# Kernel optimization log

Hardware: AMD Instinct MI355X
Metric: run time of the kernel (lower is better)

Reference implementation:

```python
import jax, jax.numpy as jnp
import numpy as np

D_MODEL = 4096
D_FF = 11008
M = 8192
GROUP = 128
NLEVELS = 16  # 4-bit


def setup_inputs() -> dict:
    key = jax.random.key(0)
    ks = jax.random.split(key, 10)
    def qw(k, K, N):
        return jax.random.randint(k, (K, N), 0, NLEVELS, dtype=jnp.int32)
    def qz(k, G, N):
        return jax.random.randint(k, (G, N), 0, NLEVELS, dtype=jnp.int32)
    def sc(k, G, N):
        # small positive per-group scales, roughly matching real AWQ magnitudes
        return jax.random.uniform(k, (G, N), dtype=jnp.float32) * 0.02 + 1e-3
    return {
        "x": jax.random.normal(ks[0], (M, D_MODEL), dtype=jnp.float32),
        "q_gate": qw(ks[1], D_MODEL, D_FF),
        "z_gate": qz(ks[2], D_MODEL // GROUP, D_FF),
        "s_gate": sc(ks[3], D_MODEL // GROUP, D_FF),
        "q_up": qw(ks[4], D_MODEL, D_FF),
        "z_up": qz(ks[5], D_MODEL // GROUP, D_FF),
        "s_up": sc(ks[6], D_MODEL // GROUP, D_FF),
        "q_down": qw(ks[7], D_FF, D_MODEL),
        "z_down": qz(ks[8], D_FF // GROUP, D_MODEL),
        "s_down": sc(ks[9], D_FF // GROUP, D_MODEL),
        "group_size": GROUP,
    }


def _dequant(q, z, s, group_size):
    # q: [K, N] int4 values; z: [K//G, N] zeros; s: [K//G, N] scales
    K, N = q.shape
    G = group_size
    w = (q.astype(s.dtype).reshape(K // G, G, N) - z.astype(s.dtype)[:, None, :]) * s[:, None, :]
    return w.reshape(K, N)


def reference(x, q_gate, z_gate, s_gate, q_up, z_up, s_up, q_down, z_down, s_down, group_size):
    gate = x @ _dequant(q_gate, z_gate, s_gate, group_size)   # [M, D_FF]
    up = x @ _dequant(q_up, z_up, s_up, group_size)           # [M, D_FF]
    h = jax.nn.silu(gate) * up                                # SwiGLU
    return h @ _dequant(q_down, z_down, s_down, group_size)   # [M, D_MODEL]
```

## Files before the change

kernel.cpp:

```cpp
#include <hip/hip_runtime.h>
#include <cstdint>

typedef unsigned short u16;
typedef unsigned int u32;
typedef unsigned char u8;
typedef signed char s8;
typedef __bf16 bf16_t;
typedef bf16_t bf16x8 __attribute__((ext_vector_type(8)));
typedef float f32x4 __attribute__((ext_vector_type(4)));
typedef int i32x4 __attribute__((ext_vector_type(4)));

#define DMODEL 4096
#define DFF 11008
#define MROWS 8192

__device__ __forceinline__ u16 f2bf(float f) {
  u32 u = __builtin_bit_cast(u32, f);
  u += 0x7FFFu + ((u >> 16) & 1u);
  return (u16)(u >> 16);
}
__device__ __forceinline__ float bf2f(u16 h) {
  return __builtin_bit_cast(float, (u32)h << 16);
}

#define GLD16(gptr, lptr)                                                  \
  __builtin_amdgcn_global_load_lds(                                        \
      (const __attribute__((address_space(1))) u32*)(gptr),                \
      (__attribute__((address_space(3))) u32*)(lptr), 16, 0, 0)

#define BAR asm volatile("s_barrier" ::: "memory")
#define VM0 asm volatile("s_waitcnt vmcnt(0)" ::: "memory")
#define VM4 asm volatile("s_waitcnt vmcnt(4)" ::: "memory")
#define LGKM0 asm volatile("s_waitcnt lgkmcnt(0)" ::: "memory")

__global__ void k_quant_x(const float* __restrict__ x, s8* __restrict__ x8,
                          float* __restrict__ sx) {
  const int row = blockIdx.x;
  const int t = threadIdx.x;
  const int lane = t & 63, wid = t >> 6;
  const float4* xr = reinterpret_cast<const float4*>(x + (size_t)row * DMODEL);
  float4 v[4];
  float m = 0.f;
#pragma unroll
  for (int i = 0; i < 4; ++i) {
    v[i] = xr[t * 4 + i];
    m = fmaxf(m, fmaxf(fmaxf(fabsf(v[i].x), fabsf(v[i].y)),
                       fmaxf(fabsf(v[i].z), fabsf(v[i].w))));
  }
#pragma unroll
  for (int off = 32; off >= 1; off >>= 1) m = fmaxf(m, __shfl_xor(m, off));
  __shared__ float wm[4];
  if (lane == 0) wm[wid] = m;
  __syncthreads();
  float mall = fmaxf(fmaxf(wm[0], wm[1]), fmaxf(wm[2], wm[3]));
  mall = fmaxf(mall, 1e-8f);
  const float inv = 127.f / mall;
  if (t == 0) sx[row] = mall / 127.f;
  uint4 o;
  u32 p[4];
#pragma unroll
  for (int i = 0; i < 4; ++i) {
    int a = (int)rintf(v[i].x * inv), b = (int)rintf(v[i].y * inv);
    int c = (int)rintf(v[i].z * inv), d = (int)rintf(v[i].w * inv);
    p[i] = (u32)(a & 255) | ((u32)(b & 255) << 8) | ((u32)(c & 255) << 16) |
           ((u32)(d & 255) << 24);
  }
  o.x = p[0]; o.y = p[1]; o.z = p[2]; o.w = p[3];
  reinterpret_cast<uint4*>(x8 + (size_t)row * DMODEL)[t] = o;
}

__global__ void k_dequant_T8(const int* __restrict__ q, const int* __restrict__ z,
                             s8* __restrict__ w8, int K, int N) {
  __shared__ s8 tile[32][40];
  const int t = threadIdx.x;
  const int n0 = blockIdx.x << 5, k0 = blockIdx.y << 5;
  {
    const int kr = t >> 3, n4 = (t & 7) << 2;
    const int k = k0 + kr, g = k >> 7;
    const int4 qv = *reinterpret_cast<const int4*>(&q[(size_t)k * N + n0 + n4]);
    const int4 zv = *reinterpret_cast<const int4*>(&z[(size_t)g * N + n0 + n4]);
    tile[kr][n4 + 0] = (s8)(qv.x - zv.x);
    tile[kr][n4 + 1] = (s8)(qv.y - zv.y);
    tile[kr][n4 + 2] = (s8)(qv.z - zv.z);
    tile[kr][n4 + 3] = (s8)(qv.w - zv.w);
  }
  __syncthreads();
  {
    const int n = t >> 3, ks = (t & 7) << 2;
    uchar4 o;
    o.x = (u8)tile[ks + 0][n];
    o.y = (u8)tile[ks + 1][n];
    o.z = (u8)tile[ks + 2][n];
    o.w = (u8)tile[ks + 3][n];
    *reinterpret_cast<uchar4*>(&w8[(size_t)(n0 + n) * K + k0 + ks]) = o;
  }
}

__global__ void k_dequant_T(const int* __restrict__ q, const int* __restrict__ z,
                            const float* __restrict__ s, u16* __restrict__ wT,
                            int K, int N) {
  __shared__ u16 tile[32][36];
  const int t = threadIdx.x;
  const int n0 = blockIdx.x << 5, k0 = blockIdx.y << 5;
  {
    const int kr = t >> 3, n4 = (t & 7) << 2;
    const int k = k0 + kr, g = k >> 7;
    const int4 qv = *reinterpret_cast<const int4*>(&q[(size_t)k * N + n0 + n4]);
    const int4 zv = *reinterpret_cast<const int4*>(&z[(size_t)g * N + n0 + n4]);
    const float4 sv = *reinterpret_cast<const float4*>(&s[(size_t)g * N + n0 + n4]);
    ushort4 o;
    o.x = f2bf((float)(qv.x - zv.x) * sv.x);
    o.y = f2bf((float)(qv.y - zv.y) * sv.y);
    o.z = f2bf((float)(qv.z - zv.z) * sv.z);
    o.w = f2bf((float)(qv.w - zv.w) * sv.w);
    *reinterpret_cast<ushort4*>(&tile[kr][n4]) = o;
  }
  __syncthreads();
  {
    const int n = t >> 3, ks = (t & 7) << 2;
    ushort4 o;
    o.x = tile[ks + 0][n];
    o.y = tile[ks + 1][n];
    o.z = tile[ks + 2][n];
    o.w = tile[ks + 3][n];
    *reinterpret_cast<ushort4*>(&wT[(size_t)(n0 + n) * K + k0 + ks]) = o;
  }
}

__global__ __launch_bounds__(512, 2) void k_fused_i8(
    const s8* __restrict__ A, const s8* __restrict__ Bg,
    const s8* __restrict__ Bu, const float* __restrict__ sx,
    const float* __restrict__ sg, const float* __restrict__ su,
    u16* __restrict__ H) {
  constexpr int Kdim = DMODEL;
  constexpr int ntiles = Kdim >> 6;
  __shared__ s8 Ab[3][256 * 64];
  __shared__ s8 Bgb[3][128 * 64];
  __shared__ s8 Bub[3][128 * 64];
  __shared__ float scl[2][32 * 128];

  const int midx = blockIdx.x & 31, nidx = blockIdx.x >> 5;
  const int m0 = midx << 8, n0 = nidx << 7;
  const int t = threadIdx.x;
  const int lane = t & 63;
  const int wid = t >> 6;
  const int wr = wid >> 2, wc = wid & 3;
  const int r16 = lane & 15, quad = lane >> 4;

  const int lrow = lane >> 2;
  const int sswz = ((lane & 3) ^ ((lrow >> 1) & 3)) << 4;
  const s8* Asrc = A + (size_t)(m0 + wid * 16 + lrow) * Kdim + sswz;
  const s8* Gsrc = Bg + (size_t)(n0 + wid * 16 + lrow) * Kdim + sswz;
  const s8* Usrc = Bu + (size_t)(n0 + wid * 16 + lrow) * Kdim + sswz;
  const size_t rstepA = (size_t)128 * Kdim;
  const int ldst = wid * 1024;

#define STG(tt, bs) do {                                                   \
    size_t ko = (size_t)((tt) & (ntiles - 1)) << 6;                        \
    GLD16(Asrc + ko,          &Ab[bs][ldst]);                              \
    GLD16(Asrc + ko + rstepA, &Ab[bs][ldst + 8192]);                       \
    GLD16(Gsrc + ko,          &Bgb[bs][ldst]);                             \
    GLD16(Usrc + ko,          &Bub[bs][ldst]);                             \
  } while (0)

  const int aswz = (quad ^ ((r16 >> 1) & 3)) << 4;
  const int abase = (wr * 128 + r16) * 64 + aswz;
  const int bbase = (wc * 32 + r16) * 64 + aswz;

  f32x4 facg[8][2], facu[8][2];
  const f32x4 zf = {0.f, 0.f, 0.f, 0.f};
#pragma unroll
  for (int mf = 0; mf < 8; ++mf)
#pragma unroll
    for (int nf = 0; nf < 2; ++nf) { facg[mf][nf] = zf; facu[mf][nf] = zf; }
  const i32x4 zi = {0, 0, 0, 0};

#pragma unroll
  for (int k = 0; k < 2; ++k) {
    int j = t + k * 512;
    int g = j >> 5;
    int c = (j & 31) << 2;
    *reinterpret_cast<float4*>(&scl[0][g * 128 + c]) =
        *reinterpret_cast<const float4*>(&sg[(size_t)g * DFF + n0 + c]);
    *reinterpret_cast<float4*>(&scl[1][g * 128 + c]) =
        *reinterpret_cast<const float4*>(&su[(size_t)g * DFF + n0 + c]);
  }
  STG(0, 0); STG(1, 1);
  VM0;
  LGKM0;
  BAR;

  const int sloc = wc * 32 + r16;

  int cur = 0;
  for (int i = 0; i < (ntiles >> 1); ++i) {
    const int a = cur;
    const int b = (a + 1 < 3) ? a + 1 : a - 2;
    const int c = (a + 2 < 3) ? a + 2 : a - 1;
    i32x4 av0[8], bg_a[2], bg_b[2], bu_a[2], bu_b[2];
#pragma unroll
    for (int mf = 0; mf < 8; ++mf)
      av0[mf] = *reinterpret_cast<const i32x4*>(&Ab[a][abase + mf * 1024]);
#pragma unroll
    for (int nf = 0; nf < 2; ++nf) {
      bg_a[nf] = *reinterpret_cast<const i32x4*>(&Bgb[a][bbase + nf * 1024]);
      bu_a[nf] = *reinterpret_cast<const i32x4*>(&Bub[a][bbase + nf * 1024]);
      bg_b[nf] = *reinterpret_cast<const i32x4*>(&Bgb[b][bbase + nf * 1024]);
      bu_b[nf] = *reinterpret_cast<const i32x4*>(&Bub[b][bbase + nf * 1024]);
    }
    float s_g0 = scl[0][i * 128 + sloc];
    float s_g1 = scl[0][i * 128 + sloc + 16];
    float s_u0 = scl[1][i * 128 + sloc];
    float s_u1 = scl[1][i * 128 + sloc + 16];
    STG(2 * i + 2, c);
    LGKM0;
    BAR;
    STG(2 * i + 3, a);
    __builtin_amdgcn_s_setprio(1);
#pragma unroll
    for (int mf = 0; mf < 8; ++mf) {
      i32x4 a1 = *reinterpret_cast<const i32x4*>(&Ab[b][abase + mf * 1024]);
      i32x4 ig0 = __builtin_amdgcn_mfma_i32_16x16x64_i8(av0[mf], bg_a[0], zi, 0, 0, 0);
      i32x4 ig1 = __builtin_amdgcn_mfma_i32_16x16x64_i8(av0[mf], bg_a[1], zi, 0, 0, 0);
      i32x4 iu0 = __builtin_amdgcn_mfma_i32_16x16x64_i8(av0[mf], bu_a[0], zi, 0, 0, 0);
      i32x4 iu1 = __builtin_amdgcn_mfma_i32_16x16x64_i8(av0[mf], bu_a[1], zi, 0, 0, 0);
      ig0 = __builtin_amdgcn_mfma_i32_16x16x64_i8(a1, bg_b[0], ig0, 0, 0, 0);
      ig1 = __builtin_amdgcn_mfma_i32_16x16x64_i8(a1, bg_b[1], ig1, 0, 0, 0);
      iu0 = __builtin_amdgcn_mfma_i32_16x16x64_i8(a1, bu_b[0], iu0, 0, 0, 0);
      iu1 = __builtin_amdgcn_mfma_i32_16x16x64_i8(a1, bu_b[1], iu1, 0, 0, 0);
#pragma unroll
      for (int j = 0; j < 4; ++j) {
        facg[mf][0][j] += (float)ig0[j] * s_g0;
        facg[mf][1][j] += (float)ig1[j] * s_g1;
        facu[mf][0][j] += (float)iu0[j] * s_u0;
        facu[mf][1][j] += (float)iu1[j] * s_u1;
      }
    }
    __builtin_amdgcn_s_setprio(0);
    VM0;
    BAR;
    cur = c;
  }

  const int rb0 = m0 + wr * 128 + quad * 4;
  const int cb0 = n0 + wc * 32 + r16;
#pragma unroll
  for (int mf = 0; mf < 8; ++mf) {
#pragma unroll
    for (int j = 0; j < 4; ++j) {
      const int row = rb0 + mf * 16 + j;
      const float sxr = sx[row];
#pragma unroll
      for (int nf = 0; nf < 2; ++nf) {
        float gv = facg[mf][nf][j] * sxr;
        float uv = facu[mf][nf][j] * sxr;
        float sv = gv / (1.f + __expf(-gv));
        H[(size_t)row * DFF + cb0 + nf * 16] = f2bf(sv * uv);
      }
    }
  }
#undef STG
}

__global__ __launch_bounds__(512, 2) void k_down(
    const u16* __restrict__ A, const u16* __restrict__ BT,
    float* __restrict__ C) {
  constexpr int Ndim = DMODEL, Kdim = DFF;
  __shared__ u16 As[2][2][256 * 32];
  __shared__ u16 Bs[2][2][256 * 32];

  const int nidx = blockIdx.x & 15;
  const int midx = blockIdx.x >> 4;
  const int m0 = midx << 8;
  const int n0 = nidx << 8;
  const int t = threadIdx.x;
  const int lane = t & 63;
  const int wid = t >> 6;
  const int wr = wid >> 2, wc = wid & 3;
  const int r16 = lane & 15, quad = lane >> 4;

  const int lrow4 = lane >> 2;
  const int sslot = ((lane & 3) ^ ((lane >> 3) & 3)) << 3;
  const u16* Asrc = A + (size_t)(m0 + wid * 16 + lrow4) * Kdim + sslot;
  const u16* Bsrc = BT + (size_t)(n0 + wid * 16 + lrow4) * Kdim + sslot;
  const size_t rstep = (size_t)128 * Kdim;
  const int lbo = wid * 512;
  constexpr int ntiles = Kdim >> 6;

#define SA(tt, kh, bf) do {                                                \
    int ttw = (tt) < ntiles ? (tt) : (tt) - ntiles;                        \
    size_t ko = ((size_t)ttw << 6) + ((kh) << 5);                          \
    GLD16(Asrc + ko,         &As[bf][kh][lbo]);                            \
    GLD16(Asrc + ko + rstep, &As[bf][kh][lbo + 4096]);                     \
  } while (0)
#define SB(tt, kh, bf) do {                                                \
    int ttw = (tt) < ntiles ? (tt) : (tt) - ntiles;                        \
    size_t ko = ((size_t)ttw << 6) + ((kh) << 5);                          \
    GLD16(Bsrc + ko,         &Bs[bf][kh][lbo]);                            \
    GLD16(Bsrc + ko + rstep, &Bs[bf][kh][lbo + 4096]);                     \
  } while (0)

  const int fragoff = (quad ^ ((r16 >> 1) & 3)) << 3;
  const int abase = (wr * 128 + r16) * 32 + fragoff;
  const int bbase = (wc * 64 + r16) * 32 + fragoff;

  f32x4 acc[8][4];
  const f32x4 zf = {0.f, 0.f, 0.f, 0.f};
#pragma unroll
  for (int mf = 0; mf < 8; ++mf)
#pragma unroll
    for (int nf = 0; nf < 4; ++nf) acc[mf][nf] = zf;

  bf16x8 avA[4], av2A[4], bvA[4];
  bf16x8 avB[4], av2B[4], bvB[4];

#define PFD(av_, av2_, bv_, bf, kk) do {                                   \
    _Pragma("unroll") for (int ii = 0; ii < 4; ++ii) {                     \
      av_[ii] = *reinterpret_cast<const bf16x8*>(                          \
          &As[bf][kk][abase + ii * 512]);                                  \
      av2_[ii] = *reinterpret_cast<const bf16x8*>(                         \
          &As[bf][kk][abase + 2048 + ii * 512]);                           \
    }                                                                      \
    _Pragma("unroll") for (int nn = 0; nn < 4; ++nn)                       \
      bv_[nn] = *reinterpret_cast<const bf16x8*>(                          \
          &Bs[bf][kk][bbase + nn * 512]);                                  \
  } while (0)

#define PHD(av_, av2_, bv_, nav_, nav2_, nbv_, STG_, VMW, bfn, kkn) do {   \
    STG_;                                                                  \
    VMW;                                                                   \
    BAR;                                                                   \
    __builtin_amdgcn_s_setprio(1);                                         \
    _Pragma("unroll") for (int ii = 0; ii < 4; ++ii)                       \
      _Pragma("unroll") for (int nn = 0; nn < 4; ++nn)                     \
        acc[ii][nn] = __builtin_amdgcn_mfma_f32_16x16x32_bf16(             \
            av_[ii], bv_[nn], acc[ii][nn], 0, 0, 0);                       \
    PFD(nav_, nav2_, nbv_, bfn, kkn);                                      \
    _Pragma("unroll") for (int ii = 0; ii < 4; ++ii)                       \
      _Pragma("unroll") for (int nn = 0; nn < 4; ++nn)                     \
        acc[4 + ii][nn] = __builtin_amdgcn_mfma_f32_16x16x32_bf16(         \
            av2_[ii], bv_[nn], acc[4 + ii][nn], 0, 0, 0);                  \
    __builtin_amdgcn_s_setprio(0);                                         \
    BAR;                                                                   \
  } while (0)

  SA(0, 0, 0); SB(0, 0, 0); SA(0, 1, 0); SB(0, 1, 0); SA(1, 0, 1); SB(1, 0, 1);
  VM4;
  BAR;
  PFD(avA, av2A, bvA, 0, 0);

  constexpr int NI = ntiles >> 1;
  for (int it = 0; it < NI; ++it) {
    const int t0 = it * 2;
    PHD(avA, av2A, bvA, avB, av2B, bvB,
        { SA(t0 + 1, 1, 1); SB(t0 + 1, 1, 1); }, (void)0, 0, 1);
    PHD(avB, av2B, bvB, avA, av2A, bvA,
        { SA(t0 + 2, 0, 0); SB(t0 + 2, 0, 0); }, VM4, 1, 0);
    PHD(avA, av2A, bvA, avB, av2B, bvB,
        { SA(t0 + 2, 1, 0); SB(t0 + 2, 1, 0); }, (void)0, 1, 1);
    PHD(avB, av2B, bvB, avA, av2A, bvA,
        { SA(t0 + 3, 0, 1); SB(t0 + 3, 0, 1); }, VM4, 0, 0);
  }
  asm volatile("s_waitcnt vmcnt(0)" ::: "memory");

  const int rb0 = m0 + wr * 128 + quad * 4;
  const int cb0 = n0 + wc * 64 + r16;
#pragma unroll
  for (int mf = 0; mf < 8; ++mf) {
#pragma unroll
    for (int nf = 0; nf < 4; ++nf) {
      f32x4 v = acc[mf][nf];
      int row = rb0 + mf * 16;
      int col = cb0 + nf * 16;
#pragma unroll
      for (int j = 0; j < 4; ++j)
        C[(size_t)(row + j) * Ndim + col] = v[j];
    }
  }
#undef SA
#undef SB
#undef PFD
#undef PHD
}

extern "C" void kernel_launch(void* const* d_in, const int* in_sizes, int n_in,
                              void* d_out, int out_size, void* d_ws, size_t ws_size,
                              hipStream_t stream) {
  const float* x  = (const float*)d_in[0];
  const int*   qg = (const int*)d_in[1];
  const int*   zg = (const int*)d_in[2];
  const float* sg = (const float*)d_in[3];
  const int*   qu = (const int*)d_in[4];
  const int*   zu = (const int*)d_in[5];
  const float* su = (const float*)d_in[6];
  const int*   qd = (const int*)d_in[7];
  const int*   zd = (const int*)d_in[8];
  const float* sd = (const float*)d_in[9];
  float* out = (float*)d_out;

  char* ws = (char*)d_ws;
  const size_t szX8 = (size_t)MROWS * DMODEL;
  const size_t szSX = (size_t)MROWS * 4;
  const size_t szW8 = (size_t)DMODEL * DFF;
  const size_t szWD = (size_t)DFF * DMODEL * 2;
  s8*    x8  = (s8*)(ws);
  float* sx  = (float*)(ws + szX8);
  s8*    wg8 = (s8*)(ws + szX8 + szSX);
  s8*    wu8 = (s8*)(ws + szX8 + szSX + szW8);
  u16*   wdT = (u16*)(ws + szX8 + szSX + 2 * szW8);
  u16*   h   = (u16*)(ws + szX8 + szSX + 2 * szW8 + szWD);

  k_quant_x<<<MROWS, 256, 0, stream>>>(x, x8, sx);
  k_dequant_T8<<<dim3(DFF / 32, DMODEL / 32), 256, 0, stream>>>(qg, zg, wg8, DMODEL, DFF);
  k_dequant_T8<<<dim3(DFF / 32, DMODEL / 32), 256, 0, stream>>>(qu, zu, wu8, DMODEL, DFF);
  k_dequant_T<<<dim3(DMODEL / 32, DFF / 32), 256, 0, stream>>>(qd, zd, sd, wdT, DFF, DMODEL);

  k_fused_i8<<<(MROWS / 256) * (DFF / 128), 512, 0, stream>>>(
      x8, wg8, wu8, sx, sg, su, h);
  k_down<<<(MROWS / 256) * (DMODEL / 256), 512, 0, stream>>>(h, wdT, out);
}
```

Before: 2.163 ms.

## Switch fused int8 gate/up kernel to double-buffered tile pairs, bf16 scales

Replaces the 3-slot rotating LDS ring with two ping-pong pairs of K-tiles. Both next tiles are issued at once, which removes the mid-iteration LGKM wait and barrier. Group scales are now stored in LDS as bf16, so the LDS footprint stays within budget for the larger 4-tile buffer. This cuts one barrier per iteration but adds bf16 rounding error on the scales and still uses a lot of LDS, which may limit occupancy.

Measured after the change: 1.824 ms. 1.19x faster.

```diff
diff --git a/kernel.cpp b/kernel.cpp
--- a/kernel.cpp
+++ b/kernel.cpp
@@ -134,10 +134,10 @@
     u16* __restrict__ H) {
   constexpr int Kdim = DMODEL;
   constexpr int ntiles = Kdim >> 6;
-  __shared__ s8 Ab[3][256 * 64];
-  __shared__ s8 Bgb[3][128 * 64];
-  __shared__ s8 Bub[3][128 * 64];
-  __shared__ float scl[2][32 * 128];
+  __shared__ s8 Ab[2][2][256 * 64];
+  __shared__ s8 Bgb[2][2][128 * 64];
+  __shared__ s8 Bub[2][2][128 * 64];
+  __shared__ u16 sclh[2][32 * 128];
 
   const int midx = blockIdx.x & 31, nidx = blockIdx.x >> 5;
   const int m0 = midx << 8, n0 = nidx << 7;
@@ -155,12 +155,12 @@
   const size_t rstepA = (size_t)128 * Kdim;
   const int ldst = wid * 1024;
 
-#define STG(tt, bs) do {                                                   \
+#define STG(tt, pb_, ti) do {                                              \
     size_t ko = (size_t)((tt) & (ntiles - 1)) << 6;                        \
-    GLD16(Asrc + ko,          &Ab[bs][ldst]);                              \
-    GLD16(Asrc + ko + rstepA, &Ab[bs][ldst + 8192]);                       \
-    GLD16(Gsrc + ko,          &Bgb[bs][ldst]);                             \
-    GLD16(Usrc + ko,          &Bub[bs][ldst]);                             \
+    GLD16(Asrc + ko,          &Ab[pb_][ti][ldst]);                         \
+    GLD16(Asrc + ko + rstepA, &Ab[pb_][ti][ldst + 8192]);                  \
+    GLD16(Gsrc + ko,          &Bgb[pb_][ti][ldst]);                        \
+    GLD16(Usrc + ko,          &Bub[pb_][ti][ldst]);                        \
   } while (0)
 
   const int aswz = (quad ^ ((r16 >> 1) & 3)) << 4;
@@ -180,46 +180,44 @@
     int j = t + k * 512;
     int g = j >> 5;
     int c = (j & 31) << 2;
-    *reinterpret_cast<float4*>(&scl[0][g * 128 + c]) =
-        *reinterpret_cast<const float4*>(&sg[(size_t)g * DFF + n0 + c]);
-    *reinterpret_cast<float4*>(&scl[1][g * 128 + c]) =
-        *reinterpret_cast<const float4*>(&su[(size_t)g * DFF + n0 + c]);
-  }
-  STG(0, 0); STG(1, 1);
+    float4 vg = *reinterpret_cast<const float4*>(&sg[(size_t)g * DFF + n0 + c]);
+    float4 vu = *reinterpret_cast<const float4*>(&su[(size_t)g * DFF + n0 + c]);
+    ushort4 og, ou;
+    og.x = f2bf(vg.x); og.y = f2bf(vg.y); og.z = f2bf(vg.z); og.w = f2bf(vg.w);
+    ou.x = f2bf(vu.x); ou.y = f2bf(vu.y); ou.z = f2bf(vu.z); ou.w = f2bf(vu.w);
+    *reinterpret_cast<ushort4*>(&sclh[0][g * 128 + c]) = og;
+    *reinterpret_cast<ushort4*>(&sclh[1][g * 128 + c]) = ou;
+  }
+  STG(0, 0, 0); STG(1, 0, 1);
   VM0;
   LGKM0;
   BAR;
 
   const int sloc = wc * 32 + r16;
 
-  int cur = 0;
   for (int i = 0; i < (ntiles >> 1); ++i) {
-    const int a = cur;
-    const int b = (a + 1 < 3) ? a + 1 : a - 2;
-    const int c = (a + 2 < 3) ? a + 2 : a - 1;
+    const int pb = i & 1;
     i32x4 av0[8], bg_a[2], bg_b[2], bu_a[2], bu_b[2];
 #pragma unroll
     for (int mf = 0; mf < 8; ++mf)
-      av0[mf] = *reinterpret_cast<const i32x4*>(&Ab[a][abase + mf * 1024]);
+      av0[mf] = *reinterpret_cast<const i32x4*>(&Ab[pb][0][abase + mf * 1024]);
 #pragma unroll
     for (int nf = 0; nf < 2; ++nf) {
-      bg_a[nf] = *reinterpret_cast<const i32x4*>(&Bgb[a][bbase + nf * 1024]);
-      bu_a[nf] = *reinterpret_cast<const i32x4*>(&Bub[a][bbase + nf * 1024]);
-      bg_b[nf] = *reinterpret_cast<const i32x4*>(&Bgb[b][bbase + nf * 1024]);
-      bu_b[nf] = *reinterpret_cast<const i32x4*>(&Bub[b][bbase + nf * 1024]);
+      bg_a[nf] = *reinterpret_cast<const i32x4*>(&Bgb[pb][0][bbase + nf * 1024]);
+      bu_a[nf] = *reinterpret_cast<const i32x4*>(&Bub[pb][0][bbase + nf * 1024]);
+      bg_b[nf] = *reinterpret_cast<const i32x4*>(&Bgb[pb][1][bbase + nf * 1024]);
+      bu_b[nf] = *reinterpret_cast<const i32x4*>(&Bub[pb][1][bbase + nf * 1024]);
     }
-    float s_g0 = scl[0][i * 128 + sloc];
-    float s_g1 = scl[0][i * 128 + sloc + 16];
-    float s_u0 = scl[1][i * 128 + sloc];
-    float s_u1 = scl[1][i * 128 + sloc + 16];
-    STG(2 * i + 2, c);
-    LGKM0;
-    BAR;
-    STG(2 * i + 3, a);
+    float s_g0 = bf2f(sclh[0][i * 128 + sloc]);
+    float s_g1 = bf2f(sclh[0][i * 128 + sloc + 16]);
+    float s_u0 = bf2f(sclh[1][i * 128 + sloc]);
+    float s_u1 = bf2f(sclh[1][i * 128 + sloc + 16]);
+    STG(2 * i + 2, pb ^ 1, 0);
+    STG(2 * i + 3, pb ^ 1, 1);
     __builtin_amdgcn_s_setprio(1);
 #pragma unroll
     for (int mf = 0; mf < 8; ++mf) {
-      i32x4 a1 = *reinterpret_cast<const i32x4*>(&Ab[b][abase + mf * 1024]);
+      i32x4 a1 = *reinterpret_cast<const i32x4*>(&Ab[pb][1][abase + mf * 1024]);
       i32x4 ig0 = __builtin_amdgcn_mfma_i32_16x16x64_i8(av0[mf], bg_a[0], zi, 0, 0, 0);
       i32x4 ig1 = __builtin_amdgcn_mfma_i32_16x16x64_i8(av0[mf], bg_a[1], zi, 0, 0, 0);
       i32x4 iu0 = __builtin_amdgcn_mfma_i32_16x16x64_i8(av0[mf], bu_a[0], zi, 0, 0, 0);
@@ -239,7 +237,6 @@
     __builtin_amdgcn_s_setprio(0);
     VM0;
     BAR;
-    cur = c;
   }
 
   const int rb0 = m0 + wr * 128 + quad * 4;
```
